# Kernel tuning notes

Hardware: AMD Instinct MI355X
Metric: run time of the kernel (lower is better)

## Reference

```python
import jax, jax.numpy as jnp
import numpy as np

# rp = [l1, l2] link parameters (stand-in for the repo's robot-parameter object)
RP = jnp.array([1.0, 1.0], dtype=jnp.float32)
EPS = 1e-8


def _mlp(x, w1, b1, w2, b2, w3, b3):
    # Linear(2,16) -> Softplus -> Linear(16,16) -> Softplus -> Linear(16,2)
    h = jax.nn.softplus(x @ w1.T + b1)
    h = jax.nn.softplus(h @ w2.T + b2)
    return h @ w3.T + b3


def _analytic_theta_0(qi):
    # smooth analytic coordinate (stand-in for transforms.analytic_theta_0)
    return RP[0] * jnp.arctan2(qi[1], qi[0])


def _analytic_theta_1(qi):
    return RP[1] * jnp.sqrt(qi[0] ** 2 + qi[1] ** 2 + EPS)


def setup_inputs() -> dict:
    key = jax.random.key(0)
    ks = jax.random.split(key, 13)
    N = 1_000_000
    q = jax.random.normal(ks[0], (N, 2), dtype=jnp.float32)

    def lin(k, out_d, in_d):
        kw, kb = jax.random.split(k)
        s = 1.0 / np.sqrt(in_d)
        w = jax.random.uniform(kw, (out_d, in_d), jnp.float32, -s, s)
        b = jax.random.uniform(kb, (out_d,), jnp.float32, -s, s)
        return w, b

    enc_w1, enc_b1 = lin(ks[1], 16, 2)
    enc_w2, enc_b2 = lin(ks[2], 16, 16)
    enc_w3, enc_b3 = lin(ks[3], 2, 16)
    dec_w1, dec_b1 = lin(ks[4], 16, 2)
    dec_w2, dec_b2 = lin(ks[5], 16, 16)
    dec_w3, dec_b3 = lin(ks[6], 2, 16)
    return dict(q=q,
                enc_w1=enc_w1, enc_b1=enc_b1, enc_w2=enc_w2, enc_b2=enc_b2,
                enc_w3=enc_w3, enc_b3=enc_b3,
                dec_w1=dec_w1, dec_b1=dec_b1, dec_w2=dec_w2, dec_b2=dec_b2,
                dec_w3=dec_w3, dec_b3=dec_b3)


def reference(q, enc_w1, enc_b1, enc_w2, enc_b2, enc_w3, enc_b3,
              dec_w1, dec_b1, dec_w2, dec_b2, dec_w3, dec_b3):
    enc = lambda x: _mlp(x, enc_w1, enc_b1, enc_w2, enc_b2, enc_w3, enc_b3)
    dec = lambda x: _mlp(x, dec_w1, dec_b1, dec_w2, dec_b2, dec_w3, dec_b3)

    # analytic jacobians (per-sample fn returns shape (1,) like unsqueeze(0))
    def f0(qi):
        t = jnp.expand_dims(_analytic_theta_0(qi), 0)
        return t, t

    def f1(qi):
        t = jnp.expand_dims(_analytic_theta_1(qi), 0)
        return t, t

    J0, _ = jax.vmap(jax.jacfwd(f0, has_aux=True))(q)  # [N,1,2]
    J1, _ = jax.vmap(jax.jacfwd(f1, has_aux=True))(q)  # [N,1,2]
    J_h_ana = jnp.concatenate([J0, J1], axis=1).astype(jnp.float32)  # [N,2,2]

    theta = enc(q)                                  # [N,2]
    J_h = jax.vmap(jax.jacfwd(enc))(q)              # [N,2,2]
    q_hat = dec(theta)                              # [N,2]
    J_h_dec = jax.vmap(jax.jacfwd(dec))(theta)      # [N,2,2]
    return theta, J_h, q_hat, J_h_dec, J_h_ana
```

## Files before the change

### kernel.cpp

```cpp
#include <hip/hip_runtime.h>
#include <math.h>


typedef float  f32x4  __attribute__((ext_vector_type(4)));
typedef short  bf16x4 __attribute__((ext_vector_type(4)));

#define LOG2E 1.44269504089f
#define LN2   0.69314718056f

__device__ __forceinline__ unsigned short f2bf1(float f) {
    unsigned u = __builtin_bit_cast(unsigned, f);
    u += 0x7FFFu + ((u >> 16) & 1u);
    return (unsigned short)(u >> 16);
}

__device__ __forceinline__ unsigned packbf(float a, float b) {
    return __builtin_amdgcn_perm(__builtin_bit_cast(unsigned, b),
                                 __builtin_bit_cast(unsigned, a), 0x07060302u);
}

__device__ __forceinline__ bf16x4 pack4(float a, float b, float c, float d) {
    union { unsigned u[2]; bf16x4 f; } x;
    x.u[0] = packbf(a, b); x.u[1] = packbf(c, d);
    return x.f;
}

__device__ __forceinline__ f32x4 mfma16(bf16x4 a, bf16x4 b, f32x4 c) {
#if __has_builtin(__builtin_amdgcn_mfma_f32_16x16x16bf16_1k)
    return __builtin_amdgcn_mfma_f32_16x16x16bf16_1k(a, b, c, 0, 0, 0);
#else
    f32x4 d;
    asm("v_mfma_f32_16x16x16_bf16 %0, %1, %2, %3"
        : "=&v"(d) : "v"(a), "v"(b), "v"(c));
    return d;
#endif
}

__device__ __forceinline__ float exp2neg(float z) {
#if __has_builtin(__builtin_amdgcn_exp2f)
    return __builtin_amdgcn_exp2f(-z);
#else
    float r; asm("v_exp_f32 %0, -%1" : "=v"(r) : "v"(z)); return r;
#endif
}

__global__ void prep_kernel(
    const float* __restrict__ ew1, const float* __restrict__ eb1,
    const float* __restrict__ ew2, const float* __restrict__ eb2,
    const float* __restrict__ ew3,
    const float* __restrict__ dw1, const float* __restrict__ db1,
    const float* __restrict__ dw2, const float* __restrict__ db2,
    const float* __restrict__ dw3,
    float* __restrict__ ws)
{
    const int t = threadIdx.x;
    if (t >= 64) return;
    const int g = t >> 4, m = t & 15;
    unsigned short* frag = (unsigned short*)(ws + 2048);
#pragma unroll
    for (int j = 0; j < 4; ++j) {
        const int i = g * 4 + j;
        const float ewa = ew1[2*i], ewb = ew1[2*i+1];
        const float dwa = dw1[2*i], dwb = dw1[2*i+1];
        ws[t*12 + j]           = ewa * LOG2E;
        ws[t*12 + 4 + j]       = ewb * LOG2E;
        ws[t*12 + 8 + j]       = eb1[i] * LOG2E;
        ws[768 + t*12 + j]     = dwa * LOG2E;
        ws[768 + t*12 + 4 + j] = dwb * LOG2E;
        ws[768 + t*12 + 8 + j] = db1[i] * LOG2E;
        ws[1536 + t*4 + j]     = eb2[i] * LOG2E;
        ws[1792 + t*4 + j]     = db2[i] * LOG2E;
        const float e2 = ew2[m*16 + i], d2 = dw2[m*16 + i];
        frag[0*256 + t*4 + j] = f2bf1(e2);
        frag[1*256 + t*4 + j] = f2bf1(e2 * ewa);
        frag[2*256 + t*4 + j] = f2bf1(e2 * ewb);
        frag[5*256 + t*4 + j] = f2bf1(d2);
        frag[6*256 + t*4 + j] = f2bf1(d2 * dwa);
        frag[7*256 + t*4 + j] = f2bf1(d2 * dwb);
        const int r3 = m & 3;
        const float e3 = (r3 < 2) ? ew3[r3*16 + i] : 0.0f;
        const float d3 = (r3 < 2) ? dw3[r3*16 + i] : 0.0f;
        frag[3*256 + t*4 + j] = f2bf1(e3 * LN2);
        frag[4*256 + t*4 + j] = f2bf1(e3);
        frag[8*256 + t*4 + j] = f2bf1(d3 * LN2);
        frag[9*256 + t*4 + j] = f2bf1(d3);
    }
}

__device__ __forceinline__ void mlp16(
    f32x4 Wa, f32x4 Wb, f32x4 Bb, f32x4 B2c,
    bf16x4 A2, bf16x4 A2a, bf16x4 A2b, bf16x4 A3v, bf16x4 A3j,
    f32x4 C3, f32x4 Z,
    float x, float y,
    float& o0, float& o1, float& J00, float& J01, float& J10, float& J11)
{
    float h0, h1, h2v, h3, s0, s1, s2, s3;
    {
        float z, t, w;
        z = fmaf(Wa[0], x, fmaf(Wb[0], y, Bb[0]));
        t = exp2neg(z); w = 1.0f + t;
        s0 = __builtin_amdgcn_rcpf(w); h0 = z + __log2f(w);
        z = fmaf(Wa[1], x, fmaf(Wb[1], y, Bb[1]));
        t = exp2neg(z); w = 1.0f + t;
        s1 = __builtin_amdgcn_rcpf(w); h1 = z + __log2f(w);
        z = fmaf(Wa[2], x, fmaf(Wb[2], y, Bb[2]));
        t = exp2neg(z); w = 1.0f + t;
        s2 = __builtin_amdgcn_rcpf(w); h2v = z + __log2f(w);
        z = fmaf(Wa[3], x, fmaf(Wb[3], y, Bb[3]));
        t = exp2neg(z); w = 1.0f + t;
        s3 = __builtin_amdgcn_rcpf(w); h3 = z + __log2f(w);
    }
    const bf16x4 Bsg = pack4(s0, s1, s2, s3);
    f32x4 zc = mfma16(A2,  pack4(h0, h1, h2v, h3), B2c);
    f32x4 ua = mfma16(A2a, Bsg, Z);
    f32x4 ub = mfma16(A2b, Bsg, Z);

    float g0, g1, g2, g3, sa0, sa1, sa2, sa3, sb0, sb1, sb2, sb3;
    {
        float t, w, r;
        t = exp2neg(zc[0]); w = 1.0f + t; r = __builtin_amdgcn_rcpf(w);
        g0 = zc[0] + __log2f(w); sa0 = r * ua[0]; sb0 = r * ub[0];
        t = exp2neg(zc[1]); w = 1.0f + t; r = __builtin_amdgcn_rcpf(w);
        g1 = zc[1] + __log2f(w); sa1 = r * ua[1]; sb1 = r * ub[1];
        t = exp2neg(zc[2]); w = 1.0f + t; r = __builtin_amdgcn_rcpf(w);
        g2 = zc[2] + __log2f(w); sa2 = r * ua[2]; sb2 = r * ub[2];
        t = exp2neg(zc[3]); w = 1.0f + t; r = __builtin_amdgcn_rcpf(w);
        g3 = zc[3] + __log2f(w); sa3 = r * ua[3]; sb3 = r * ub[3];
    }
    f32x4 oz = mfma16(A3v, pack4(g0,  g1,  g2,  g3),  C3);
    f32x4 oa = mfma16(A3j, pack4(sa0, sa1, sa2, sa3), Z);
    f32x4 ob = mfma16(A3j, pack4(sb0, sb1, sb2, sb3), Z);
    o0 = oz[0]; o1 = oz[1];
    J00 = oa[0]; J10 = oa[1]; J01 = ob[0]; J11 = ob[1];
}

__global__ __launch_bounds__(256, 4) void ae_mfma_kernel(
    const float* __restrict__ q,
    const float* __restrict__ eb3, const float* __restrict__ db3,
    const float* __restrict__ ws, float* __restrict__ out, int n)
{
    const int lane = threadIdx.x & 63;
    const int wv = blockIdx.x * 4 + (threadIdx.x >> 6);
    const int g = lane >> 4, m16 = lane & 15;
    const long base = (long)wv * 64;
    if (base >= n) return;

    const f32x4 eWa = *(const f32x4*)(ws + (size_t)lane*12);
    const f32x4 eWb = *(const f32x4*)(ws + (size_t)lane*12 + 4);
    const f32x4 eBb = *(const f32x4*)(ws + (size_t)lane*12 + 8);
    const f32x4 dWa = *(const f32x4*)(ws + 768 + (size_t)lane*12);
    const f32x4 dWb = *(const f32x4*)(ws + 768 + (size_t)lane*12 + 4);
    const f32x4 dBb = *(const f32x4*)(ws + 768 + (size_t)lane*12 + 8);
    const f32x4 eB2 = *(const f32x4*)(ws + 1536 + (size_t)lane*4);
    const f32x4 dB2 = *(const f32x4*)(ws + 1792 + (size_t)lane*4);
    const bf16x4* fr = (const bf16x4*)(ws + 2048);
    const bf16x4 A2e  = fr[0*64 + lane], A2ae = fr[1*64 + lane];
    const bf16x4 A2be = fr[2*64 + lane];
    const bf16x4 A3ve = fr[3*64 + lane], A3je = fr[4*64 + lane];
    const bf16x4 A2d  = fr[5*64 + lane], A2ad = fr[6*64 + lane];
    const bf16x4 A2bd = fr[7*64 + lane];
    const bf16x4 A3vd = fr[8*64 + lane], A3jd = fr[9*64 + lane];
    f32x4 C3e; C3e[0] = eb3[0]; C3e[1] = eb3[1]; C3e[2] = 0.0f; C3e[3] = 0.0f;
    f32x4 C3d; C3d[0] = db3[0]; C3d[1] = db3[1]; C3d[2] = 0.0f; C3d[3] = 0.0f;
    f32x4 Z;   Z[0] = 0.0f; Z[1] = 0.0f; Z[2] = 0.0f; Z[3] = 0.0f;

    const size_t nn = (size_t)n;

#define LOADXY(c, xc, yc)                                                   \
    float xc, yc;                                                           \
    {                                                                       \
        long s_ = base + (c)*16 + m16;                                      \
        long si_ = s_ < n ? s_ : (long)n - 1;                               \
        const float2 qv_ = ((const float2*)q)[si_];                         \
        xc = qv_.x; yc = qv_.y;                                             \
    }

#define ENC(c, xc, yc)                                                      \
    float t0_##c, t1_##c, E00_##c, E01_##c, E10_##c, E11_##c;               \
    mlp16(eWa, eWb, eBb, eB2, A2e, A2ae, A2be, A3ve, A3je, C3e, Z, xc, yc,  \
          t0_##c, t1_##c, E00_##c, E01_##c, E10_##c, E11_##c);

#define DEC_STORE(c)                                                        \
    {                                                                       \
        float q0_, q1_, D00_, D01_, D10_, D11_;                             \
        mlp16(dWa, dWb, dBb, dB2, A2d, A2ad, A2bd, A3vd, A3jd, C3d, Z,      \
              t0_##c, t1_##c, q0_, q1_, D00_, D01_, D10_, D11_);            \
        long sp_ = base + (c)*16 + m16;                                     \
        if (g == (c) && sp_ < n) {                                          \
            const float2 qv_ = ((const float2*)q)[sp_];                     \
            const float xc = qv_.x, yc = qv_.y;                             \
            float r2_ = fmaf(xc, xc, yc * yc);                              \
            float iv_ = __builtin_amdgcn_rcpf(r2_);                         \
            float rv_ = __builtin_amdgcn_rsqf(r2_ + 1e-8f);                 \
            ((float2*)(out))[sp_]          = make_float2(t0_##c, t1_##c);   \
            ((float4*)(out + 2*nn))[sp_]   = make_float4(E00_##c, E01_##c,  \
                                                         E10_##c, E11_##c); \
            ((float2*)(out + 6*nn))[sp_]   = make_float2(q0_, q1_);         \
            ((float4*)(out + 8*nn))[sp_]   = make_float4(D00_, D01_,        \
                                                         D10_, D11_);       \
            ((float4*)(out + 12*nn))[sp_]  = make_float4(-yc * iv_, xc * iv_,\
                                                         xc * rv_, yc * rv_);\
        }                                                                   \
    }

    LOADXY(0, x0, y0) LOADXY(1, x1, y1) LOADXY(2, x2, y2) LOADXY(3, x3, y3)

    ENC(0, x0, y0)
    ENC(1, x1, y1)
    ENC(2, x2, y2)
    ENC(3, x3, y3)
    DEC_STORE(0)
    DEC_STORE(1)
    DEC_STORE(2)
    DEC_STORE(3)

#undef LOADXY
#undef ENC
#undef DEC_STORE
}

extern "C" void kernel_launch(void* const* d_in, const int* in_sizes, int n_in,
                              void* d_out, int out_size, void* d_ws, size_t ws_size,
                              hipStream_t stream)
{
    const float* q   = (const float*)d_in[0];
    const float* ew1 = (const float*)d_in[1];
    const float* eb1 = (const float*)d_in[2];
    const float* ew2 = (const float*)d_in[3];
    const float* eb2 = (const float*)d_in[4];
    const float* ew3 = (const float*)d_in[5];
    const float* eb3 = (const float*)d_in[6];
    const float* dw1 = (const float*)d_in[7];
    const float* db1 = (const float*)d_in[8];
    const float* dw2 = (const float*)d_in[9];
    const float* db2 = (const float*)d_in[10];
    const float* dw3 = (const float*)d_in[11];
    const float* db3 = (const float*)d_in[12];

    const int n = in_sizes[0] / 2;
    float* ws = (float*)d_ws;

    prep_kernel<<<1, 64, 0, stream>>>(ew1, eb1, ew2, eb2, ew3,
                                      dw1, db1, dw2, db2, dw3, ws);

    const int waves  = (n + 63) / 64;
    const int blocks = (waves + 3) / 4;
    ae_mfma_kernel<<<blocks, 256, 0, stream>>>(q, eb3, db3, ws, (float*)d_out, n);
}
```

Before: 121.0 us.

## Fold weight prep into main kernel and use persistent grid-stride loop

```diff
diff --git a/kernel.cpp b/kernel.cpp
--- a/kernel.cpp
+++ b/kernel.cpp
@@ -42,49 +42,6 @@
 #else
     float r; asm("v_exp_f32 %0, -%1" : "=v"(r) : "v"(z)); return r;
 #endif
-}
-
-__global__ void prep_kernel(
-    const float* __restrict__ ew1, const float* __restrict__ eb1,
-    const float* __restrict__ ew2, const float* __restrict__ eb2,
-    const float* __restrict__ ew3,
-    const float* __restrict__ dw1, const float* __restrict__ db1,
-    const float* __restrict__ dw2, const float* __restrict__ db2,
-    const float* __restrict__ dw3,
-    float* __restrict__ ws)
-{
-    const int t = threadIdx.x;
-    if (t >= 64) return;
-    const int g = t >> 4, m = t & 15;
-    unsigned short* frag = (unsigned short*)(ws + 2048);
-#pragma unroll
-    for (int j = 0; j < 4; ++j) {
-        const int i = g * 4 + j;
-        const float ewa = ew1[2*i], ewb = ew1[2*i+1];
-        const float dwa = dw1[2*i], dwb = dw1[2*i+1];
-        ws[t*12 + j]           = ewa * LOG2E;
-        ws[t*12 + 4 + j]       = ewb * LOG2E;
-        ws[t*12 + 8 + j]       = eb1[i] * LOG2E;
-        ws[768 + t*12 + j]     = dwa * LOG2E;
-        ws[768 + t*12 + 4 + j] = dwb * LOG2E;
-        ws[768 + t*12 + 8 + j] = db1[i] * LOG2E;
-        ws[1536 + t*4 + j]     = eb2[i] * LOG2E;
-        ws[1792 + t*4 + j]     = db2[i] * LOG2E;
-        const float e2 = ew2[m*16 + i], d2 = dw2[m*16 + i];
-        frag[0*256 + t*4 + j] = f2bf1(e2);
-        frag[1*256 + t*4 + j] = f2bf1(e2 * ewa);
-        frag[2*256 + t*4 + j] = f2bf1(e2 * ewb);
-        frag[5*256 + t*4 + j] = f2bf1(d2);
-        frag[6*256 + t*4 + j] = f2bf1(d2 * dwa);
-        frag[7*256 + t*4 + j] = f2bf1(d2 * dwb);
-        const int r3 = m & 3;
-        const float e3 = (r3 < 2) ? ew3[r3*16 + i] : 0.0f;
-        const float d3 = (r3 < 2) ? dw3[r3*16 + i] : 0.0f;
-        frag[3*256 + t*4 + j] = f2bf1(e3 * LN2);
-        frag[4*256 + t*4 + j] = f2bf1(e3);
-        frag[8*256 + t*4 + j] = f2bf1(d3 * LN2);
-        frag[9*256 + t*4 + j] = f2bf1(d3);
-    }
 }
 
 __device__ __forceinline__ void mlp16(
@@ -136,35 +93,50 @@
 
 __global__ __launch_bounds__(256, 4) void ae_mfma_kernel(
     const float* __restrict__ q,
-    const float* __restrict__ eb3, const float* __restrict__ db3,
-    const float* __restrict__ ws, float* __restrict__ out, int n)
+    const float* __restrict__ ew1, const float* __restrict__ eb1,
+    const float* __restrict__ ew2, const float* __restrict__ eb2,
+    const float* __restrict__ ew3, const float* __restrict__ eb3,
+    const float* __restrict__ dw1, const float* __restrict__ db1,
+    const float* __restrict__ dw2, const float* __restrict__ db2,
+    const float* __restrict__ dw3, const float* __restrict__ db3,
+    float* __restrict__ out, int n)
 {
     const int lane = threadIdx.x & 63;
-    const int wv = blockIdx.x * 4 + (threadIdx.x >> 6);
     const int g = lane >> 4, m16 = lane & 15;
-    const long base = (long)wv * 64;
-    if (base >= n) return;
-
-    const f32x4 eWa = *(const f32x4*)(ws + (size_t)lane*12);
-    const f32x4 eWb = *(const f32x4*)(ws + (size_t)lane*12 + 4);
-    const f32x4 eBb = *(const f32x4*)(ws + (size_t)lane*12 + 8);
-    const f32x4 dWa = *(const f32x4*)(ws + 768 + (size_t)lane*12);
-    const f32x4 dWb = *(const f32x4*)(ws + 768 + (size_t)lane*12 + 4);
-    const f32x4 dBb = *(const f32x4*)(ws + 768 + (size_t)lane*12 + 8);
-    const f32x4 eB2 = *(const f32x4*)(ws + 1536 + (size_t)lane*4);
-    const f32x4 dB2 = *(const f32x4*)(ws + 1792 + (size_t)lane*4);
-    const bf16x4* fr = (const bf16x4*)(ws + 2048);
-    const bf16x4 A2e  = fr[0*64 + lane], A2ae = fr[1*64 + lane];
-    const bf16x4 A2be = fr[2*64 + lane];
-    const bf16x4 A3ve = fr[3*64 + lane], A3je = fr[4*64 + lane];
-    const bf16x4 A2d  = fr[5*64 + lane], A2ad = fr[6*64 + lane];
-    const bf16x4 A2bd = fr[7*64 + lane];
-    const bf16x4 A3vd = fr[8*64 + lane], A3jd = fr[9*64 + lane];
+
+    f32x4 eWa, eWb, eBb, dWa, dWb, dBb, eB2, dB2;
+    bf16x4 A2e, A2ae, A2be, A3ve, A3je, A2d, A2ad, A2bd, A3vd, A3jd;
+#pragma unroll
+    for (int j = 0; j < 4; ++j) {
+        const int i = g * 4 + j;
+        const float ewa = ew1[2*i], ewb = ew1[2*i+1];
+        const float dwa = dw1[2*i], dwb = dw1[2*i+1];
+        eWa[j] = ewa * LOG2E;  eWb[j] = ewb * LOG2E;  eBb[j] = eb1[i] * LOG2E;
+        dWa[j] = dwa * LOG2E;  dWb[j] = dwb * LOG2E;  dBb[j] = db1[i] * LOG2E;
+        eB2[j] = eb2[i] * LOG2E;  dB2[j] = db2[i] * LOG2E;
+        const float e2 = ew2[m16*16 + i], d2 = dw2[m16*16 + i];
+        A2e[j]  = (short)f2bf1(e2);
+        A2ae[j] = (short)f2bf1(e2 * ewa);
+        A2be[j] = (short)f2bf1(e2 * ewb);
+        A2d[j]  = (short)f2bf1(d2);
+        A2ad[j] = (short)f2bf1(d2 * dwa);
+        A2bd[j] = (short)f2bf1(d2 * dwb);
+        const int r3 = m16 & 3;
+        const float e3 = (r3 < 2) ? ew3[r3*16 + i] : 0.0f;
+        const float d3 = (r3 < 2) ? dw3[r3*16 + i] : 0.0f;
+        A3ve[j] = (short)f2bf1(e3 * LN2);
+        A3je[j] = (short)f2bf1(e3);
+        A3vd[j] = (short)f2bf1(d3 * LN2);
+        A3jd[j] = (short)f2bf1(d3);
+    }
     f32x4 C3e; C3e[0] = eb3[0]; C3e[1] = eb3[1]; C3e[2] = 0.0f; C3e[3] = 0.0f;
     f32x4 C3d; C3d[0] = db3[0]; C3d[1] = db3[1]; C3d[2] = 0.0f; C3d[3] = 0.0f;
     f32x4 Z;   Z[0] = 0.0f; Z[1] = 0.0f; Z[2] = 0.0f; Z[3] = 0.0f;
 
     const size_t nn = (size_t)n;
+    const long nwav = ((long)n + 63) >> 6;
+    const long wv0 = (long)blockIdx.x * 4 + (threadIdx.x >> 6);
+    const long stride = (long)gridDim.x * 4;
 
 #define LOADXY(c, xc, yc)                                                   \
     float xc, yc;                                                           \
@@ -203,16 +175,21 @@
         }                                                                   \
     }
 
-    LOADXY(0, x0, y0) LOADXY(1, x1, y1) LOADXY(2, x2, y2) LOADXY(3, x3, y3)
-
-    ENC(0, x0, y0)
-    ENC(1, x1, y1)
-    ENC(2, x2, y2)
-    ENC(3, x3, y3)
-    DEC_STORE(0)
-    DEC_STORE(1)
-    DEC_STORE(2)
-    DEC_STORE(3)
+    for (long wv = wv0; wv < nwav; wv += stride) {
+        const long base = wv * 64;
+
+        LOADXY(0, x0, y0) LOADXY(1, x1, y1)
+        LOADXY(2, x2, y2) LOADXY(3, x3, y3)
+
+        ENC(0, x0, y0)
+        ENC(1, x1, y1)
+        ENC(2, x2, y2)
+        ENC(3, x3, y3)
+        DEC_STORE(0)
+        DEC_STORE(1)
+        DEC_STORE(2)
+        DEC_STORE(3)
+    }
 
 #undef LOADXY
 #undef ENC
@@ -238,12 +215,13 @@
     const float* db3 = (const float*)d_in[12];
 
     const int n = in_sizes[0] / 2;
-    float* ws = (float*)d_ws;
-
-    prep_kernel<<<1, 64, 0, stream>>>(ew1, eb1, ew2, eb2, ew3,
-                                      dw1, db1, dw2, db2, dw3, ws);
-
-    const int waves  = (n + 63) / 64;
-    const int blocks = (waves + 3) / 4;
-    ae_mfma_kernel<<<blocks, 256, 0, stream>>>(q, eb3, db3, ws, (float*)d_out, n);
-}
+
+    const long nwav = ((long)n + 63) >> 6;
+    long blocks = (nwav + 3) / 4;
+    if (blocks > 1024) blocks = 1024;
+    if (blocks < 1) blocks = 1;
+
+    ae_mfma_kernel<<<(int)blocks, 256, 0, stream>>>(
+        q, ew1, eb1, ew2, eb2, ew3, eb3,
+        dw1, db1, dw2, db2, dw3, db3, (float*)d_out, n);
+}
```

Result: slower. 124.2 us (+2.6%).
